# Kernel tuning notes

Measured on AMD Instinct MI355X. Metric: run time of the kernel, lower is better.

Reference implementation:

```python
import jax, jax.numpy as jnp
from jax import lax
import numpy as np

NEG = jnp.float32(-1e9)


def monotonic_alignment_search(logp, text_lengths, mel_lengths):
    """Glow-TTS style MAS. logp: [B, Tt, Tm] (log_softmax over text axis).
    Returns integer durations [B, Tt] summing to mel_lengths per batch."""
    B, Tt, Tm = logp.shape
    i_range = jnp.arange(Tt)
    text_mask = i_range[None, :] < text_lengths[:, None]            # [B, Tt]
    logp = jnp.where(text_mask[:, :, None], logp, NEG)

    # ---- forward DP over mel frames: Q[i,j] = logp[i,j] + max(Q[i,j-1], Q[i-1,j-1])
    q0 = jnp.where(i_range[None, :] == 0, logp[:, :, 0], NEG)        # [B, Tt]

    def fwd(q, lp_j):
        q_shift = jnp.concatenate([jnp.full((B, 1), NEG), q[:, :-1]], axis=1)
        take_diag = q_shift > q                                      # came from i-1
        q_new = lp_j + jnp.maximum(q, q_shift)
        return q_new, take_diag

    _, choices = lax.scan(fwd, q0, jnp.moveaxis(logp[:, :, 1:], 2, 0))  # [Tm-1, B, Tt]
    choices = jnp.concatenate([jnp.zeros((1, B, Tt), bool), choices], axis=0)  # align j

    # ---- backtrack from (text_len-1, mel_len-1) down to j=0
    b_idx = jnp.arange(B)

    def bwd(i, j):
        active = j < mel_lengths                                     # [B]
        dur_inc = (active[:, None] & (i_range[None, :] == i[:, None]))
        ch = choices[j, b_idx, i]                                    # [B] bool
        i_new = jnp.where(active & (j > 0), i - ch.astype(i.dtype), i)
        return i_new, dur_inc

    i0 = text_lengths - 1
    _, durs = lax.scan(bwd, i0, jnp.arange(Tm - 1, -1, -1))
    return durs.sum(0).astype(jnp.int32)                             # [B, Tt]


def length_regulate(h_text, durations, mel_lengths, Tm):
    """Expand h_text [B,Tt,D] by durations [B,Tt] to [B,Tm,D]."""
    B, Tt, D = h_text.shape
    cum = jnp.cumsum(durations, axis=1)                              # [B, Tt]
    j = jnp.arange(Tm)
    idx = (cum[:, None, :] <= j[None, :, None]).sum(-1)              # [B, Tm]
    idx = jnp.clip(idx, 0, Tt - 1)
    h_exp = jnp.take_along_axis(h_text, idx[:, :, None], axis=1)     # [B, Tm, D]
    mel_mask = j[None, :] < mel_lengths[:, None]
    return h_exp * mel_mask[:, :, None].astype(h_exp.dtype)


def setup_inputs() -> dict:
    B, Tt, Tm, D, M = 32, 512, 2048, 512, 80
    k = jax.random.split(jax.random.key(0), 6)
    return {
        "h_text": jax.random.normal(k[0], (B, Tt, D), jnp.float32),
        "mel": jax.random.normal(k[1], (B, M, Tm), jnp.float32),
        "text_lengths": jax.random.randint(k[2], (B,), 256, Tt + 1, jnp.int32),
        "mel_lengths": jax.random.randint(k[3], (B,), 1024, Tm + 1, jnp.int32),
        "w_proj": jax.random.normal(k[4], (D, M), jnp.float32) * 0.02,
        "b_proj": jnp.zeros((D,), jnp.float32),
        "log_dur_pred": jax.random.normal(k[5], (B, Tt), jnp.float32) * 0.5,
    }


def reference(h_text, mel, text_lengths, mel_lengths, w_proj, b_proj, log_dur_pred):
    B, Tt, D = h_text.shape
    Tm = mel.shape[2]

    # mel_proj = Linear(n_mels -> d_model) on mel.transpose(1,2)
    mel_proj = jnp.einsum('bmt,dm->btd', mel, w_proj) + b_proj       # [B, Tm, D]

    # alignment scores + masked log_softmax over text axis
    attn = jnp.einsum('btd,bsd->bts', h_text, mel_proj)              # [B, Tt, Tm]
    text_mask = jnp.arange(Tt)[None, :] >= text_lengths[:, None]
    mel_mask = jnp.arange(Tm)[None, :] >= mel_lengths[:, None]
    attn = jnp.where(text_mask[:, :, None], NEG, attn)
    attn = jnp.where(mel_mask[:, None, :], NEG, attn)
    logp = jax.nn.log_softmax(attn, axis=1)

    durations = monotonic_alignment_search(logp, text_lengths, mel_lengths)

    # duration loss (masked sum-MSE in log domain)
    dur_mask = (jnp.arange(Tt)[None, :] < text_lengths[:, None]).astype(jnp.float32)
    log_dur_gt = jnp.log(jnp.clip(durations.astype(jnp.float32), 1.0, None))
    diff = log_dur_pred * dur_mask - log_dur_gt * dur_mask
    dur_loss = jnp.sum(diff * diff) / jnp.sum(dur_mask)

    h_expanded = length_regulate(h_text, durations, mel_lengths, Tm)  # [B, Tm, D]
    return (h_expanded, dur_loss, durations)
```

## Files before the change

### kernel.cpp

```cpp
#include <hip/hip_runtime.h>
#include <math.h>

#define Bn 32
#define TT 512
#define TM 2048
#define DD 512
#define MMp 80
#define NEGF (-1.0e9f)

constexpr size_t LOSS_OFF = (size_t)Bn * TM * DD;
constexpr size_t DUR_OFF  = LOSS_OFF + 1;

__global__ __launch_bounds__(256) void k0_wtx(const float* __restrict__ w,
                                              const float* __restrict__ bias,
                                              float* __restrict__ wTx) {
    int m = blockIdx.x;
    for (int d = threadIdx.x; d < DD; d += 256) {
        float v = 0.f;
        if (m < 80) v = w[d * 80 + m];
        else if (m == 80) v = bias[d];
        wTx[m * DD + d] = v;
    }
}

__global__ __launch_bounds__(256) void k1_hw(const float* __restrict__ h_text,
                                             const float* __restrict__ wTx,
                                             float* __restrict__ hwX) {
    int bid = blockIdx.x;
    int b = bid >> 3;
    int i0 = (bid & 7) * 64;
    int t = threadIdx.x;
    int tr = t & 15, tc = t >> 4;
    __shared__ __align__(16) float Asub[64 * 68];
    __shared__ __align__(16) float Bsub[96 * 68];
    float acc[4][6];
#pragma unroll
    for (int a = 0; a < 4; ++a)
#pragma unroll
        for (int c = 0; c < 6; ++c) acc[a][c] = 0.f;

    for (int d0 = 0; d0 < DD; d0 += 64) {
        __syncthreads();
#pragma unroll
        for (int p = 0; p < 4; ++p) {
            int lin = p * 256 + t;
            int r = lin >> 4, dq = lin & 15;
            *(float4*)&Asub[r * 68 + dq * 4] =
                *(const float4*)&h_text[((size_t)(b * TT + i0 + r)) * DD + d0 + dq * 4];
        }
#pragma unroll
        for (int p = 0; p < 6; ++p) {
            int lin = p * 256 + t;
            int cc = lin >> 4, dq = lin & 15;
            *(float4*)&Bsub[cc * 68 + dq * 4] =
                *(const float4*)&wTx[(size_t)cc * DD + d0 + dq * 4];
        }
        __syncthreads();
#pragma unroll
        for (int dd = 0; dd < 16; ++dd) {
            float4 a[4], bb[6];
#pragma unroll
            for (int ri = 0; ri < 4; ++ri)
                a[ri] = *(const float4*)&Asub[(tr * 4 + ri) * 68 + dd * 4];
#pragma unroll
            for (int ci = 0; ci < 6; ++ci)
                bb[ci] = *(const float4*)&Bsub[(tc * 6 + ci) * 68 + dd * 4];
#pragma unroll
            for (int ri = 0; ri < 4; ++ri)
#pragma unroll
                for (int ci = 0; ci < 6; ++ci) {
                    acc[ri][ci] += a[ri].x * bb[ci].x;
                    acc[ri][ci] += a[ri].y * bb[ci].y;
                    acc[ri][ci] += a[ri].z * bb[ci].z;
                    acc[ri][ci] += a[ri].w * bb[ci].w;
                }
        }
    }
#pragma unroll
    for (int ri = 0; ri < 4; ++ri)
#pragma unroll
        for (int ci = 0; ci < 6; ++ci)
            hwX[((size_t)b * 96 + tc * 6 + ci) * DD + i0 + tr * 4 + ri] = acc[ri][ci];
}

__global__ __launch_bounds__(256) void k2_attn(const float* __restrict__ hwX,
                                               const float* __restrict__ mel,
                                               const int* __restrict__ tlen,
                                               const int* __restrict__ mlen,
                                               float* __restrict__ logpT) {
    const int b = blockIdx.y;
    const int ml = mlen[b];
    const int j0 = blockIdx.x * 32;
    if (j0 >= ml) return;
    const int tl = tlen[b];
    const int tid = threadIdx.x;
    const int ig = tid >> 2;
    const int jg = tid & 3;

    __shared__ __align__(16) float hwS[16 * 512];
    __shared__ __align__(16) float melS[16 * 32];
    __shared__ float red[32 * 64];
    __shared__ float colmax[32];
    __shared__ float lsum[32];

    float acc[8][8];
#pragma unroll
    for (int a = 0; a < 8; ++a)
#pragma unroll
        for (int c = 0; c < 8; ++c) acc[a][c] = 0.f;

    for (int mc = 0; mc < 80; mc += 16) {
        __syncthreads();
#pragma unroll
        for (int p = 0; p < 8; ++p) {
            int lin = p * 256 + tid;
            int mm = lin >> 7, iq = lin & 127;
            *(float4*)&hwS[mm * 512 + iq * 4] =
                *(const float4*)&hwX[((size_t)b * 96 + mc + mm) * DD + iq * 4];
        }
#pragma unroll
        for (int p = 0; p < 2; ++p) {
            int lin = p * 256 + tid;
            int mm = lin >> 5, jj = lin & 31;
            melS[lin] = mel[((size_t)b * 80 + mc + mm) * TM + j0 + jj];
        }
        __syncthreads();
#pragma unroll
        for (int mm = 0; mm < 16; ++mm) {
            float4 a0 = *(const float4*)&hwS[mm * 512 + ig * 8];
            float4 a1 = *(const float4*)&hwS[mm * 512 + ig * 8 + 4];
            float4 b0 = *(const float4*)&melS[mm * 32 + jg * 8];
            float4 b1 = *(const float4*)&melS[mm * 32 + jg * 8 + 4];
            float av[8] = {a0.x, a0.y, a0.z, a0.w, a1.x, a1.y, a1.z, a1.w};
            float bv[8] = {b0.x, b0.y, b0.z, b0.w, b1.x, b1.y, b1.z, b1.w};
#pragma unroll
            for (int ii = 0; ii < 8; ++ii)
#pragma unroll
                for (int jj = 0; jj < 8; ++jj) acc[ii][jj] += av[ii] * bv[jj];
        }
    }
    float4 h0 = *(const float4*)&hwX[((size_t)b * 96 + 80) * DD + ig * 8];
    float4 h1 = *(const float4*)&hwX[((size_t)b * 96 + 80) * DD + ig * 8 + 4];
    float hb[8] = {h0.x, h0.y, h0.z, h0.w, h1.x, h1.y, h1.z, h1.w};
#pragma unroll
    for (int ii = 0; ii < 8; ++ii) {
        bool valid = (ig * 8 + ii) < tl;
#pragma unroll
        for (int jj = 0; jj < 8; ++jj)
            acc[ii][jj] = valid ? (acc[ii][jj] + hb[ii]) : NEGF;
    }
    __syncthreads();
#pragma unroll
    for (int jj = 0; jj < 8; ++jj) {
        float m = acc[0][jj];
#pragma unroll
        for (int ii = 1; ii < 8; ++ii) m = fmaxf(m, acc[ii][jj]);
        red[(jg * 8 + jj) * 64 + ig] = m;
    }
    __syncthreads();
    if (tid < 32) {
        float m = red[tid * 64];
        for (int g = 1; g < 64; ++g) m = fmaxf(m, red[tid * 64 + g]);
        colmax[tid] = m;
    }
    __syncthreads();
#pragma unroll
    for (int jj = 0; jj < 8; ++jj) {
        float cm = colmax[jg * 8 + jj];
        float s = 0.f;
#pragma unroll
        for (int ii = 0; ii < 8; ++ii) s += expf(acc[ii][jj] - cm);
        red[(jg * 8 + jj) * 64 + ig] = s;
    }
    __syncthreads();
    if (tid < 32) {
        float s = 0.f;
        for (int g = 0; g < 64; ++g) s += red[tid * 64 + g];
        lsum[tid] = logf(s);
    }
    __syncthreads();
#pragma unroll
    for (int jj = 0; jj < 8; ++jj) {
        int j = j0 + jg * 8 + jj;
        if (j < ml) {
            float cm = colmax[jg * 8 + jj], ls = lsum[jg * 8 + jj];
            float o[8];
#pragma unroll
            for (int ii = 0; ii < 8; ++ii) {
                int i = ig * 8 + ii;
                o[ii] = (i < tl) ? ((acc[ii][jj] - cm) - ls) : NEGF;
            }
            float* dst = &logpT[((size_t)b * TM + j) * TT + ig * 8];
            *(float4*)dst = make_float4(o[0], o[1], o[2], o[3]);
            *(float4*)(dst + 4) = make_float4(o[4], o[5], o[6], o[7]);
        }
    }
}

#define BCOLS 15
#define NBATCH 137

__device__ __forceinline__ void lds_dma16(const float* g, float* l) {
    __builtin_amdgcn_global_load_lds((const __attribute__((address_space(1))) void*)g,
                                     (__attribute__((address_space(3))) void*)l,
                                     16, 0, 0);
}
#define WAITALL  asm volatile("s_waitcnt vmcnt(0)" ::: "memory")
#define WAITLGKM asm volatile("s_waitcnt lgkmcnt(0)" ::: "memory")

__device__ __forceinline__ float dpp_shr1(float old, float src) {
    return __int_as_float(__builtin_amdgcn_update_dpp(
        __float_as_int(old), __float_as_int(src), 0x138, 0xF, 0xF, false));
}

__global__ __launch_bounds__(64, 1) void k3_dp(const float* __restrict__ logpT,
                                               const int* __restrict__ tlen,
                                               const int* __restrict__ mlen,
                                               unsigned* __restrict__ gwords,
                                               int* __restrict__ idxmap,
                                               float* __restrict__ dOut) {
    const int b = blockIdx.x;
    const int lane = threadIdx.x;
    const int tl = tlen[b];
    const int ml = mlen[b];
    __shared__ __align__(16) float ring0[BCOLS * 512];
    __shared__ __align__(16) float ring1[BCOLS * 512];
    __shared__ int durs[TT];
#pragma unroll
    for (int k = 0; k < 8; ++k) durs[lane * 8 + k] = 0;

    const float* colbase = logpT + (size_t)b * TM * TT;
    unsigned* gwb = gwords + (size_t)b * TT * 64;

    float q[8];
    unsigned accb[8];
#pragma unroll
    for (int k = 0; k < 8; ++k) { q[k] = NEGF; accb[k] = 0u; }
    if (lane == 0) q[0] = colbase[0];

    {
        const float* g0 = colbase + (size_t)512 + lane * 4;
#pragma unroll
        for (int p = 0; p < BCOLS; ++p) {
            lds_dma16(g0 + p * 512,       &ring0[p * 512]);
            lds_dma16(g0 + p * 512 + 256, &ring0[p * 512 + 256]);
        }
    }
    WAITALL;

    unsigned* gp = gwb + lane * 8 * 64;
    int jj = 1;
    for (int n = 0; n < NBATCH; ++n) {
        const float* bufc = (n & 1) ? ring1 : ring0;
        float* bufn = (n & 1) ? ring0 : ring1;
        float4 ra[BCOLS], rb[BCOLS];
#pragma unroll
        for (int p = 0; p < BCOLS; ++p) {
            ra[p] = *(const float4*)&bufc[p * 512 + lane * 8];
            rb[p] = *(const float4*)&bufc[p * 512 + lane * 8 + 4];
        }
        WAITLGKM;
        if (n + 1 < NBATCH) {
            const int jb = 1 + (n + 1) * BCOLS;
#pragma unroll
            for (int p = 0; p < BCOLS; ++p) {
                int c = jb + p;
                c = (c > TM - 1) ? (TM - 1) : c;
                const float* g = colbase + (size_t)c * 512 + lane * 4;
                lds_dma16(g,       &bufn[p * 512]);
                lds_dma16(g + 256, &bufn[p * 512 + 256]);
            }
        }
#pragma unroll
        for (int p = 0; p < BCOLS; ++p) {
            float lp[8] = {ra[p].x, ra[p].y, ra[p].z, ra[p].w,
                           rb[p].x, rb[p].y, rb[p].z, rb[p].w};
            float nb[8];
            nb[0] = dpp_shr1(NEGF, q[7]);
#pragma unroll
            for (int k = 1; k < 8; ++k) nb[k] = q[k - 1];
            const unsigned m32 = 1u << (jj & 31);
#pragma unroll
            for (int k = 0; k < 8; ++k) {
                if (nb[k] > q[k]) accb[k] |= m32;
                q[k] = lp[k] + fmaxf(q[k], nb[k]);
            }
            if ((jj & 31) == 31) {
#pragma unroll
                for (int k = 0; k < 8; ++k) { gp[k * 64] = accb[k]; accb[k] = 0u; }
                gp += 1;
            }
            ++jj;
        }
        WAITALL;
    }
    __threadfence();
    __syncthreads();

    {
        int i = tl - 1;
        int j = ml - 1;
        unsigned r0, r1, r2, r3, r4, r5, r6, r7;
        {
            int a0 = tl - 1, a1 = tl - 2, a2 = tl - 3, a3 = tl - 4;
            int a4 = tl - 5, a5 = tl - 6, a6 = tl - 7, a7 = tl - 8;
            a1 = a1 < 0 ? 0 : a1; a2 = a2 < 0 ? 0 : a2; a3 = a3 < 0 ? 0 : a3;
            a4 = a4 < 0 ? 0 : a4; a5 = a5 < 0 ? 0 : a5; a6 = a6 < 0 ? 0 : a6;
            a7 = a7 < 0 ? 0 : a7;
            r0 = gwb[a0 * 64 + lane]; r1 = gwb[a1 * 64 + lane];
            r2 = gwb[a2 * 64 + lane]; r3 = gwb[a3 * 64 + lane];
            r4 = gwb[a4 * 64 + lane]; r5 = gwb[a5 * 64 + lane];
            r6 = gwb[a6 * 64 + lane]; r7 = gwb[a7 * 64 + lane];
        }
        int nf = tl - 9;
        int guard = TT + 2;
        while (guard-- > 0) {
            unsigned w = r0;
            r0 = r1; r1 = r2; r2 = r3; r3 = r4; r4 = r5; r5 = r6; r6 = r7;
            {
                int rf = (nf < 0) ? 0 : nf;
                r7 = gwb[rf * 64 + lane];
                --nf;
            }
            int jw = j >> 5, rr = j & 31;
            unsigned topmask = (rr == 31) ? 0xFFFFFFFFu : ((1u << (rr + 1)) - 1u);
            unsigned wm = (lane < jw) ? w : ((lane == jw) ? (w & topmask) : 0u);
            unsigned long long bal = __ballot(wm != 0u);
            if (bal == 0ull) {
                if (lane == 0) durs[i] = j + 1;
                break;
            }
            int hl = 63 - __clzll(bal);
            unsigned whl = (unsigned)__builtin_amdgcn_readlane((int)wm, hl);
            int jp = (hl << 5) + (31 - __clz(whl));
            if (lane == 0) durs[i] = j - jp + 1;
            j = jp - 1;
            if (--i < 0) break;
        }
    }
    __syncthreads();

    int d[8], pre[8];
    int run = 0;
#pragma unroll
    for (int k = 0; k < 8; ++k) { d[k] = durs[lane * 8 + k]; pre[k] = run; run += d[k]; }
    int v = run;
#pragma unroll
    for (int off = 1; off < 64; off <<= 1) {
        int n = __shfl_up(v, off);
        if (lane >= off) v += n;
    }
    int base = v - run;
#pragma unroll
    for (int k = 0; k < 8; ++k) {
        int i = lane * 8 + k;
        dOut[DUR_OFF + (size_t)b * TT + i] = (float)d[k];
        int st = base + pre[k];
        for (int t2 = 0; t2 < d[k]; ++t2) idxmap[b * TM + st + t2] = i;
    }
}

__global__ __launch_bounds__(128) void k4_expand(const float* __restrict__ h_text,
                                                 const int* __restrict__ idxmap,
                                                 const int* __restrict__ mlen,
                                                 float* __restrict__ dOut) {
    int bid = blockIdx.x;
    int b = bid >> 11;
    int j = bid & (TM - 1);
    int t = threadIdx.x;
    float4* orow = (float4*)dOut + (size_t)bid * 128;
    if (j < mlen[b]) {
        int i = idxmap[bid];
        const float4* hrow = (const float4*)h_text + ((size_t)(b * TT + i)) * 128;
        orow[t] = hrow[t];
    } else {
        orow[t] = make_float4(0.f, 0.f, 0.f, 0.f);
    }
}

__global__ __launch_bounds__(256) void k5_loss(const float* __restrict__ pred,
                                               const int* __restrict__ tlen,
                                               float* __restrict__ dOut) {
    __shared__ float rs[256];
    __shared__ int rc[256];
    int t = threadIdx.x;
    float s = 0.f;
    int c = 0;
    for (int idx = t; idx < Bn * TT; idx += 256) {
        int b = idx >> 9, i = idx & 511;
        if (i < tlen[b]) {
            float dv = dOut[DUR_OFF + idx];
            float lg = logf(fmaxf(dv, 1.0f));
            float df = pred[idx] - lg;
            s += df * df;
            c += 1;
        }
    }
    rs[t] = s; rc[t] = c;
    __syncthreads();
    for (int off = 128; off > 0; off >>= 1) {
        if (t < off) { rs[t] += rs[t + off]; rc[t] += rc[t + off]; }
        __syncthreads();
    }
    if (t == 0) dOut[LOSS_OFF] = rs[0] / (float)rc[0];
}

extern "C" void kernel_launch(void* const* d_in, const int* in_sizes, int n_in,
                              void* d_out, int out_size, void* d_ws, size_t ws_size,
                              hipStream_t stream) {
    const float* h_text = (const float*)d_in[0];
    const float* mel    = (const float*)d_in[1];
    const int*   tlen   = (const int*)d_in[2];
    const int*   mlen   = (const int*)d_in[3];
    const float* w      = (const float*)d_in[4];
    const float* bias   = (const float*)d_in[5];
    const float* pred   = (const float*)d_in[6];
    float* out = (float*)d_out;

    float*    logpT  = (float*)d_ws;
    float*    hwX    = logpT + (size_t)Bn * TM * TT;
    float*    wTx    = hwX + (size_t)Bn * 96 * DD;
    unsigned* gwords = (unsigned*)(wTx + 96 * DD);
    int*      idxmap = (int*)(gwords + (size_t)Bn * TT * 64);

    k0_wtx<<<dim3(96), dim3(256), 0, stream>>>(w, bias, wTx);
    k1_hw<<<dim3(256), dim3(256), 0, stream>>>(h_text, wTx, hwX);
    k2_attn<<<dim3(64, 32), dim3(256), 0, stream>>>(hwX, mel, tlen, mlen, logpT);
    k3_dp<<<dim3(32), dim3(64), 0, stream>>>(logpT, tlen, mlen, gwords, idxmap, out);
    k4_expand<<<dim3(Bn * TM), dim3(128), 0, stream>>>(h_text, idxmap, mlen, out);
    k5_loss<<<dim3(1), dim3(256), 0, stream>>>(pred, tlen, out);
}
```

Baseline: 827.9 us.

## Replace LDS DMA double buffer with register triple-buffered global loads in DP

The forward DP kernel used to stage logp columns through two LDS ring buffers filled by global_load_lds DMA, with explicit vmcnt and lgkmcnt waits. It now loads each column batch straight from global memory into three rotating register buffers, issuing two batches ahead of the one being consumed, with 8 columns per batch instead of 15. This removes the LDS round trip and the full vmcnt wait at the end of every batch, so the serial recurrence should stall less on memory. In exchange register pressure rises, and the old clamp on column indices is gone, so prefetches run past column TM-1 into the next batch's data or past the end of the buffer for the last batch.

```diff
diff --git a/kernel.cpp b/kernel.cpp
--- a/kernel.cpp
+++ b/kernel.cpp
@@ -197,16 +197,8 @@
     }
 }
 
-#define BCOLS 15
-#define NBATCH 137
-
-__device__ __forceinline__ void lds_dma16(const float* g, float* l) {
-    __builtin_amdgcn_global_load_lds((const __attribute__((address_space(1))) void*)g,
-                                     (__attribute__((address_space(3))) void*)l,
-                                     16, 0, 0);
-}
-#define WAITALL  asm volatile("s_waitcnt vmcnt(0)" ::: "memory")
-#define WAITLGKM asm volatile("s_waitcnt lgkmcnt(0)" ::: "memory")
+#define BCOLS 8
+#define NBATCH 258
 
 __device__ __forceinline__ float dpp_shr1(float old, float src) {
     return __int_as_float(__builtin_amdgcn_update_dpp(
@@ -223,8 +215,6 @@
     const int lane = threadIdx.x;
     const int tl = tlen[b];
     const int ml = mlen[b];
-    __shared__ __align__(16) float ring0[BCOLS * 512];
-    __shared__ __align__(16) float ring1[BCOLS * 512];
     __shared__ int durs[TT];
 #pragma unroll
     for (int k = 0; k < 8; ++k) durs[lane * 8 + k] = 0;
@@ -238,62 +228,60 @@
     for (int k = 0; k < 8; ++k) { q[k] = NEGF; accb[k] = 0u; }
     if (lane == 0) q[0] = colbase[0];
 
-    {
-        const float* g0 = colbase + (size_t)512 + lane * 4;
-#pragma unroll
-        for (int p = 0; p < BCOLS; ++p) {
-            lds_dma16(g0 + p * 512,       &ring0[p * 512]);
-            lds_dma16(g0 + p * 512 + 256, &ring0[p * 512 + 256]);
-        }
-    }
-    WAITALL;
-
     unsigned* gp = gwb + lane * 8 * 64;
     int jj = 1;
-    for (int n = 0; n < NBATCH; ++n) {
-        const float* bufc = (n & 1) ? ring1 : ring0;
-        float* bufn = (n & 1) ? ring0 : ring1;
-        float4 ra[BCOLS], rb[BCOLS];
-#pragma unroll
-        for (int p = 0; p < BCOLS; ++p) {
-            ra[p] = *(const float4*)&bufc[p * 512 + lane * 8];
-            rb[p] = *(const float4*)&bufc[p * 512 + lane * 8 + 4];
-        }
-        WAITLGKM;
-        if (n + 1 < NBATCH) {
-            const int jb = 1 + (n + 1) * BCOLS;
-#pragma unroll
-            for (int p = 0; p < BCOLS; ++p) {
-                int c = jb + p;
-                c = (c > TM - 1) ? (TM - 1) : c;
-                const float* g = colbase + (size_t)c * 512 + lane * 4;
-                lds_dma16(g,       &bufn[p * 512]);
-                lds_dma16(g + 256, &bufn[p * 512 + 256]);
-            }
-        }
-#pragma unroll
-        for (int p = 0; p < BCOLS; ++p) {
-            float lp[8] = {ra[p].x, ra[p].y, ra[p].z, ra[p].w,
-                           rb[p].x, rb[p].y, rb[p].z, rb[p].w};
-            float nb[8];
-            nb[0] = dpp_shr1(NEGF, q[7]);
-#pragma unroll
-            for (int k = 1; k < 8; ++k) nb[k] = q[k - 1];
-            const unsigned m32 = 1u << (jj & 31);
-#pragma unroll
-            for (int k = 0; k < 8; ++k) {
-                if (nb[k] > q[k]) accb[k] |= m32;
-                q[k] = lp[k] + fmaxf(q[k], nb[k]);
-            }
-            if ((jj & 31) == 31) {
-#pragma unroll
-                for (int k = 0; k < 8; ++k) { gp[k * 64] = accb[k]; accb[k] = 0u; }
-                gp += 1;
-            }
-            ++jj;
-        }
-        WAITALL;
-    }
+    const float* lanebase = colbase + lane * 8;
+
+    float4 ra0[BCOLS], rb0[BCOLS], ra1[BCOLS], rb1[BCOLS], ra2[BCOLS], rb2[BCOLS];
+
+#define ISSUE(nb_, ra_, rb_) do {                                              \
+        const float* g_ = lanebase + ((size_t)(1 + (nb_) * BCOLS)) * 512;      \
+        _Pragma("unroll")                                                      \
+        for (int p_ = 0; p_ < BCOLS; ++p_) {                                   \
+            ra_[p_] = *(const float4*)(g_ + (size_t)p_ * 512);                 \
+            rb_[p_] = *(const float4*)(g_ + (size_t)p_ * 512 + 4);             \
+        }                                                                      \
+    } while (0)
+
+#define STEPS(ra_, rb_) do {                                                   \
+        _Pragma("unroll")                                                      \
+        for (int p_ = 0; p_ < BCOLS; ++p_) {                                   \
+            float lp_[8] = {ra_[p_].x, ra_[p_].y, ra_[p_].z, ra_[p_].w,        \
+                            rb_[p_].x, rb_[p_].y, rb_[p_].z, rb_[p_].w};       \
+            float nb_[8];                                                      \
+            nb_[0] = dpp_shr1(NEGF, q[7]);                                     \
+            _Pragma("unroll")                                                  \
+            for (int k_ = 1; k_ < 8; ++k_) nb_[k_] = q[k_ - 1];                \
+            const unsigned m32_ = 1u << (jj & 31);                             \
+            _Pragma("unroll")                                                  \
+            for (int k_ = 0; k_ < 8; ++k_) {                                   \
+                if (nb_[k_] > q[k_]) accb[k_] |= m32_;                         \
+                q[k_] = lp_[k_] + fmaxf(q[k_], nb_[k_]);                       \
+            }                                                                  \
+            if ((jj & 31) == 31) {                \
+                _Pragma("unroll")                                              \
+                for (int k_ = 0; k_ < 8; ++k_) {                               \
+                    gp[k_ * 64] = accb[k_]; accb[k_] = 0u;                     \
+                }                                                              \
+                gp += 1;                                                       \
+            }                                                                  \
+            ++jj;                                                              \
+        }                                                                      \
+    } while (0)
+
+    ISSUE(0, ra0, rb0);
+    ISSUE(1, ra1, rb1);
+    for (int n = 0; n < NBATCH; n += 3) {
+        ISSUE(n + 2, ra2, rb2);
+        STEPS(ra0, rb0);
+        ISSUE(n + 3, ra0, rb0);
+        STEPS(ra1, rb1);
+        ISSUE(n + 4, ra1, rb1);
+        STEPS(ra2, rb2);
+    }
+#undef ISSUE
+#undef STEPS
+
     __threadfence();
     __syncthreads();
 
```

Measured after the change: 752.6 us. 1.1x faster.

## Split MAS DP into producer wave for LDS prefetch and compute wave

Applied to the files above, without the earlier changes.

The DP kernel now runs two waves per batch. One wave issues global-to-LDS DMA loads for the next 16 columns while the other does the forward recurrence. Each compute lane now owns rows split as two groups of 4 (lane*4 and 256+lane*4), with a DPP rotate to carry the boundary between the halves. The aim is to take memory waits off the serial DP critical path, at the cost of a __syncthreads per 16-column block. The backtrack and idxmap writes also gain bounds clamping, and k4 masks the index.

```diff
diff --git a/kernel.cpp b/kernel.cpp
--- a/kernel.cpp
+++ b/kernel.cpp
@@ -197,166 +197,184 @@
     }
 }
 
-#define BCOLS 15
-#define NBATCH 137
+#define KVB 16
+#define NKB 128
+
+typedef float vf4 __attribute__((ext_vector_type(4)));
 
 __device__ __forceinline__ void lds_dma16(const float* g, float* l) {
     __builtin_amdgcn_global_load_lds((const __attribute__((address_space(1))) void*)g,
                                      (__attribute__((address_space(3))) void*)l,
                                      16, 0, 0);
 }
-#define WAITALL  asm volatile("s_waitcnt vmcnt(0)" ::: "memory")
-#define WAITLGKM asm volatile("s_waitcnt lgkmcnt(0)" ::: "memory")
 
 __device__ __forceinline__ float dpp_shr1(float old, float src) {
     return __int_as_float(__builtin_amdgcn_update_dpp(
         __float_as_int(old), __float_as_int(src), 0x138, 0xF, 0xF, false));
 }
-
-__global__ __launch_bounds__(64, 1) void k3_dp(const float* __restrict__ logpT,
-                                               const int* __restrict__ tlen,
-                                               const int* __restrict__ mlen,
-                                               unsigned* __restrict__ gwords,
-                                               int* __restrict__ idxmap,
-                                               float* __restrict__ dOut) {
+__device__ __forceinline__ float dpp_ror1(float src) {
+    return __int_as_float(__builtin_amdgcn_update_dpp(
+        __float_as_int(src), __float_as_int(src), 0x13C, 0xF, 0xF, false));
+}
+
+__global__ __launch_bounds__(128, 1) void k3_dp(const float* __restrict__ logpT,
+                                                const int* __restrict__ tlen,
+                                                const int* __restrict__ mlen,
+                                                unsigned* __restrict__ gwords,
+                                                int* __restrict__ idxmap,
+                                                float* __restrict__ dOut) {
     const int b = blockIdx.x;
-    const int lane = threadIdx.x;
+    const int tid = threadIdx.x;
+    const int wid = tid >> 6;
+    const int lane = tid & 63;
     const int tl = tlen[b];
     const int ml = mlen[b];
-    __shared__ __align__(16) float ring0[BCOLS * 512];
-    __shared__ __align__(16) float ring1[BCOLS * 512];
+
+    __shared__ __align__(16) float ring[2][KVB][512];
     __shared__ int durs[TT];
-#pragma unroll
-    for (int k = 0; k < 8; ++k) durs[lane * 8 + k] = 0;
+    for (int idx = tid; idx < TT; idx += 128) durs[idx] = 0;
 
     const float* colbase = logpT + (size_t)b * TM * TT;
     unsigned* gwb = gwords + (size_t)b * TT * 64;
 
-    float q[8];
-    unsigned accb[8];
-#pragma unroll
-    for (int k = 0; k < 8; ++k) { q[k] = NEGF; accb[k] = 0u; }
-    if (lane == 0) q[0] = colbase[0];
-
-    {
-        const float* g0 = colbase + (size_t)512 + lane * 4;
-#pragma unroll
-        for (int p = 0; p < BCOLS; ++p) {
-            lds_dma16(g0 + p * 512,       &ring0[p * 512]);
-            lds_dma16(g0 + p * 512 + 256, &ring0[p * 512 + 256]);
-        }
-    }
-    WAITALL;
-
-    unsigned* gp = gwb + lane * 8 * 64;
+    if (wid == 1) {
+        const float* src0 = colbase + (size_t)512 + lane * 4;
+#pragma unroll
+        for (int c = 0; c < KVB; ++c) {
+            lds_dma16(src0 + c * 512,       &ring[0][c][0]);
+            lds_dma16(src0 + c * 512 + 256, &ring[0][c][256]);
+        }
+    }
+
+    float qa[4], qb[4];
+    unsigned accA[4], accB[4];
+#pragma unroll
+    for (int k = 0; k < 4; ++k) { qa[k] = NEGF; qb[k] = NEGF; accA[k] = 0u; accB[k] = 0u; }
+    if (wid == 0 && lane == 0) qa[0] = colbase[0];
+    unsigned* gpA = gwb + (size_t)(4 * lane) * 64;
+    unsigned* gpB = gwb + (size_t)(256 + 4 * lane) * 64;
+    int woff = 0;
     int jj = 1;
-    for (int n = 0; n < NBATCH; ++n) {
-        const float* bufc = (n & 1) ? ring1 : ring0;
-        float* bufn = (n & 1) ? ring0 : ring1;
-        float4 ra[BCOLS], rb[BCOLS];
-#pragma unroll
-        for (int p = 0; p < BCOLS; ++p) {
-            ra[p] = *(const float4*)&bufc[p * 512 + lane * 8];
-            rb[p] = *(const float4*)&bufc[p * 512 + lane * 8 + 4];
-        }
-        WAITLGKM;
-        if (n + 1 < NBATCH) {
-            const int jb = 1 + (n + 1) * BCOLS;
-#pragma unroll
-            for (int p = 0; p < BCOLS; ++p) {
-                int c = jb + p;
-                c = (c > TM - 1) ? (TM - 1) : c;
-                const float* g = colbase + (size_t)c * 512 + lane * 4;
-                lds_dma16(g,       &bufn[p * 512]);
-                lds_dma16(g + 256, &bufn[p * 512 + 256]);
+    const int lane4 = lane * 4;
+
+    __syncthreads();
+
+    for (int kb = 0; kb < NKB; ++kb) {
+        if (wid == 1) {
+            if (kb + 1 < NKB) {
+                const int j0 = 1 + (kb + 1) * KVB;
+                const float* src = colbase + (size_t)j0 * 512 + lane * 4;
+                float* slot = &ring[(kb + 1) & 1][0][0];
+#pragma unroll
+                for (int c = 0; c < KVB; ++c) {
+                    lds_dma16(src + c * 512,       slot + c * 512);
+                    lds_dma16(src + c * 512 + 256, slot + c * 512 + 256);
+                }
             }
-        }
-#pragma unroll
-        for (int p = 0; p < BCOLS; ++p) {
-            float lp[8] = {ra[p].x, ra[p].y, ra[p].z, ra[p].w,
-                           rb[p].x, rb[p].y, rb[p].z, rb[p].w};
-            float nb[8];
-            nb[0] = dpp_shr1(NEGF, q[7]);
-#pragma unroll
-            for (int k = 1; k < 8; ++k) nb[k] = q[k - 1];
-            const unsigned m32 = 1u << (jj & 31);
-#pragma unroll
-            for (int k = 0; k < 8; ++k) {
-                if (nb[k] > q[k]) accb[k] |= m32;
-                q[k] = lp[k] + fmaxf(q[k], nb[k]);
+        } else {
+            const float* slab = &ring[kb & 1][0][0];
+#pragma unroll
+            for (int c = 0; c < KVB; ++c) {
+                vf4 la = *(const vf4*)&slab[c * 512 + lane4];
+                vf4 lb = *(const vf4*)&slab[c * 512 + 256 + lane4];
+                float wrap = dpp_ror1(qa[3]);
+                float nA0 = dpp_shr1(NEGF, qa[3]);
+                float nB0 = dpp_shr1(wrap, qb[3]);
+                float nA[4], nB[4];
+                nA[0] = nA0; nB[0] = nB0;
+#pragma unroll
+                for (int k = 1; k < 4; ++k) { nA[k] = qa[k - 1]; nB[k] = qb[k - 1]; }
+                const unsigned m32 = 1u << (jj & 31);
+                float lpA[4] = {la[0], la[1], la[2], la[3]};
+                float lpB[4] = {lb[0], lb[1], lb[2], lb[3]};
+#pragma unroll
+                for (int k = 0; k < 4; ++k) {
+                    if (nA[k] > qa[k]) accA[k] |= m32;
+                    qa[k] = lpA[k] + fmaxf(qa[k], nA[k]);
+                    if (nB[k] > qb[k]) accB[k] |= m32;
+                    qb[k] = lpB[k] + fmaxf(qb[k], nB[k]);
+                }
+                if ((jj & 31) == 31) {
+#pragma unroll
+                    for (int k = 0; k < 4; ++k) {
+                        gpA[k * 64 + woff] = accA[k]; accA[k] = 0u;
+                        gpB[k * 64 + woff] = accB[k]; accB[k] = 0u;
+                    }
+                    ++woff;
+                }
+                ++jj;
             }
-            if ((jj & 31) == 31) {
-#pragma unroll
-                for (int k = 0; k < 8; ++k) { gp[k * 64] = accb[k]; accb[k] = 0u; }
-                gp += 1;
+        }
+        __syncthreads();
+    }
+
+    __threadfence();
+    __syncthreads();
+
+    if (wid == 0) {
+        {
+            int i = tl - 1;
+            int j = ml - 1;
+            unsigned r0, r1, r2, r3, r4, r5, r6, r7;
+            {
+                int a0 = tl - 1, a1 = tl - 2, a2 = tl - 3, a3 = tl - 4;
+                int a4 = tl - 5, a5 = tl - 6, a6 = tl - 7, a7 = tl - 8;
+                a1 = a1 < 0 ? 0 : a1; a2 = a2 < 0 ? 0 : a2; a3 = a3 < 0 ? 0 : a3;
+                a4 = a4 < 0 ? 0 : a4; a5 = a5 < 0 ? 0 : a5; a6 = a6 < 0 ? 0 : a6;
+                a7 = a7 < 0 ? 0 : a7;
+                r0 = gwb[a0 * 64 + lane]; r1 = gwb[a1 * 64 + lane];
+                r2 = gwb[a2 * 64 + lane]; r3 = gwb[a3 * 64 + lane];
+                r4 = gwb[a4 * 64 + lane]; r5 = gwb[a5 * 64 + lane];
+                r6 = gwb[a6 * 64 + lane]; r7 = gwb[a7 * 64 + lane];
             }
-            ++jj;
-        }
-        WAITALL;
-    }
-    __threadfence();
-    __syncthreads();
-
-    {
-        int i = tl - 1;
-        int j = ml - 1;
-        unsigned r0, r1, r2, r3, r4, r5, r6, r7;
-        {
-            int a0 = tl - 1, a1 = tl - 2, a2 = tl - 3, a3 = tl - 4;
-            int a4 = tl - 5, a5 = tl - 6, a6 = tl - 7, a7 = tl - 8;
-            a1 = a1 < 0 ? 0 : a1; a2 = a2 < 0 ? 0 : a2; a3 = a3 < 0 ? 0 : a3;
-            a4 = a4 < 0 ? 0 : a4; a5 = a5 < 0 ? 0 : a5; a6 = a6 < 0 ? 0 : a6;
-            a7 = a7 < 0 ? 0 : a7;
-            r0 = gwb[a0 * 64 + lane]; r1 = gwb[a1 * 64 + lane];
-            r2 = gwb[a2 * 64 + lane]; r3 = gwb[a3 * 64 + lane];
-            r4 = gwb[a4 * 64 + lane]; r5 = gwb[a5 * 64 + lane];
-            r6 = gwb[a6 * 64 + lane]; r7 = gwb[a7 * 64 + lane];
-        }
-        int nf = tl - 9;
-        int guard = TT + 2;
-        while (guard-- > 0) {
-            unsigned w = r0;
-            r0 = r1; r1 = r2; r2 = r3; r3 = r4; r4 = r5; r5 = r6; r6 = r7;
-            {
-                int rf = (nf < 0) ? 0 : nf;
-                r7 = gwb[rf * 64 + lane];
-                --nf;
+            int nf = tl - 9;
+            int guard = TT + 2;
+            while (guard-- > 0) {
+                unsigned w = r0;
+                r0 = r1; r1 = r2; r2 = r3; r3 = r4; r4 = r5; r5 = r6; r6 = r7;
+                {
+                    int rf = (nf < 0) ? 0 : nf;
+                    r7 = gwb[rf * 64 + lane];
+                    --nf;
+                }
+                int jw = j >> 5, rr = j & 31;
+                unsigned topmask = (rr == 31) ? 0xFFFFFFFFu : ((1u << (rr + 1)) - 1u);
+                unsigned wm = (lane < jw) ? w : ((lane == jw) ? (w & topmask) : 0u);
+                unsigned long long bal = __ballot(wm != 0u);
+                if (bal == 0ull) {
+                    if (lane == 0) durs[i] = j + 1;
+                    break;
+                }
+                int hl = 63 - __clzll(bal);
+                unsigned whl = (unsigned)__builtin_amdgcn_readlane((int)wm, hl);
+                int jp = (hl << 5) + (31 - __clz(whl));
+                if (lane == 0) durs[i] = j - jp + 1;
+                j = jp - 1;
+                if (--i < 0) break;
             }
-            int jw = j >> 5, rr = j & 31;
-            unsigned topmask = (rr == 31) ? 0xFFFFFFFFu : ((1u << (rr + 1)) - 1u);
-            unsigned wm = (lane < jw) ? w : ((lane == jw) ? (w & topmask) : 0u);
-            unsigned long long bal = __ballot(wm != 0u);
-            if (bal == 0ull) {
-                if (lane == 0) durs[i] = j + 1;
-                break;
-            }
-            int hl = 63 - __clzll(bal);
-            unsigned whl = (unsigned)__builtin_amdgcn_readlane((int)wm, hl);
-            int jp = (hl << 5) + (31 - __clz(whl));
-            if (lane == 0) durs[i] = j - jp + 1;
-            j = jp - 1;
-            if (--i < 0) break;
-        }
-    }
-    __syncthreads();
-
-    int d[8], pre[8];
-    int run = 0;
-#pragma unroll
-    for (int k = 0; k < 8; ++k) { d[k] = durs[lane * 8 + k]; pre[k] = run; run += d[k]; }
-    int v = run;
-#pragma unroll
-    for (int off = 1; off < 64; off <<= 1) {
-        int n = __shfl_up(v, off);
-        if (lane >= off) v += n;
-    }
-    int base = v - run;
-#pragma unroll
-    for (int k = 0; k < 8; ++k) {
-        int i = lane * 8 + k;
-        dOut[DUR_OFF + (size_t)b * TT + i] = (float)d[k];
-        int st = base + pre[k];
-        for (int t2 = 0; t2 < d[k]; ++t2) idxmap[b * TM + st + t2] = i;
+        }
+
+        int d[8], pre[8];
+        int run = 0;
+#pragma unroll
+        for (int k = 0; k < 8; ++k) { d[k] = durs[lane * 8 + k]; pre[k] = run; run += d[k]; }
+        int v = run;
+#pragma unroll
+        for (int off = 1; off < 64; off <<= 1) {
+            int n = __shfl_up(v, off);
+            if (lane >= off) v += n;
+        }
+        int base = v - run;
+#pragma unroll
+        for (int k = 0; k < 8; ++k) {
+            int i = lane * 8 + k;
+            dOut[DUR_OFF + (size_t)b * TT + i] = (float)d[k];
+            int st = base + pre[k];
+            int en = st + d[k];
+            if (en > TM) en = TM;
+            if (st < 0) st = 0;
+            for (int t2 = st; t2 < en; ++t2) idxmap[b * TM + t2] = i;
+        }
     }
 }
 
@@ -370,7 +388,7 @@
     int t = threadIdx.x;
     float4* orow = (float4*)dOut + (size_t)bid * 128;
     if (j < mlen[b]) {
-        int i = idxmap[bid];
+        int i = idxmap[bid] & (TT - 1);
         const float4* hrow = (const float4*)h_text + ((size_t)(b * TT + i)) * 128;
         orow[t] = hrow[t];
     } else {
@@ -426,7 +444,7 @@
     k0_wtx<<<dim3(96), dim3(256), 0, stream>>>(w, bias, wTx);
     k1_hw<<<dim3(256), dim3(256), 0, stream>>>(h_text, wTx, hwX);
     k2_attn<<<dim3(64, 32), dim3(256), 0, stream>>>(hwX, mel, tlen, mlen, logpT);
-    k3_dp<<<dim3(32), dim3(64), 0, stream>>>(logpT, tlen, mlen, gwords, idxmap, out);
+    k3_dp<<<dim3(32), dim3(128), 0, stream>>>(logpT, tlen, mlen, gwords, idxmap, out);
     k4_expand<<<dim3(Bn * TM), dim3(128), 0, stream>>>(h_text, idxmap, mlen, out);
     k5_loss<<<dim3(1), dim3(256), 0, stream>>>(pred, tlen, out);
 }
```

Result: no change. 829.5 us (+0.2%).

## Rotate DP across three wavefronts with register-prefetched column chunks

Applied to the files above, without the earlier changes.

The serial MAS forward DP kernel now runs three wavefronts per batch. Each wavefront owns every third chunk of 16 mel columns and prefetches its next chunk straight into registers with global loads, replacing the LDS DMA ring. The DP state (q and partial choice bits) is handed between waves through shared memory, with a block barrier after each chunk, so memory latency is hidden by the other waves' loads. This adds a barrier and an LDS state round trip per chunk, and clamps the idxmap range and index as safety.

```diff
diff --git a/kernel.cpp b/kernel.cpp
--- a/kernel.cpp
+++ b/kernel.cpp
@@ -197,166 +197,179 @@
     }
 }
 
-#define BCOLS 15
-#define NBATCH 137
-
-__device__ __forceinline__ void lds_dma16(const float* g, float* l) {
-    __builtin_amdgcn_global_load_lds((const __attribute__((address_space(1))) void*)g,
-                                     (__attribute__((address_space(3))) void*)l,
-                                     16, 0, 0);
-}
-#define WAITALL  asm volatile("s_waitcnt vmcnt(0)" ::: "memory")
-#define WAITLGKM asm volatile("s_waitcnt lgkmcnt(0)" ::: "memory")
+#define KC3 16
+#define NB3 128
+#define K3T 192
+
+typedef float vf4 __attribute__((ext_vector_type(4)));
+typedef unsigned vu4 __attribute__((ext_vector_type(4)));
+
+#define SB0() __builtin_amdgcn_sched_barrier(0)
 
 __device__ __forceinline__ float dpp_shr1(float old, float src) {
     return __int_as_float(__builtin_amdgcn_update_dpp(
         __float_as_int(old), __float_as_int(src), 0x138, 0xF, 0xF, false));
 }
 
-__global__ __launch_bounds__(64, 1) void k3_dp(const float* __restrict__ logpT,
-                                               const int* __restrict__ tlen,
-                                               const int* __restrict__ mlen,
-                                               unsigned* __restrict__ gwords,
-                                               int* __restrict__ idxmap,
-                                               float* __restrict__ dOut) {
+__global__ __launch_bounds__(K3T, 1) void k3_dp(const float* __restrict__ logpT,
+                                                const int* __restrict__ tlen,
+                                                const int* __restrict__ mlen,
+                                                unsigned* __restrict__ gwords,
+                                                int* __restrict__ idxmap,
+                                                float* __restrict__ dOut) {
     const int b = blockIdx.x;
-    const int lane = threadIdx.x;
+    const int tid = threadIdx.x;
+    const int wid = tid >> 6;
+    const int lane = tid & 63;
     const int tl = tlen[b];
     const int ml = mlen[b];
-    __shared__ __align__(16) float ring0[BCOLS * 512];
-    __shared__ __align__(16) float ring1[BCOLS * 512];
+
+    __shared__ __align__(16) float qs[TT];
+    __shared__ __align__(16) unsigned as2[TT];
     __shared__ int durs[TT];
-#pragma unroll
-    for (int k = 0; k < 8; ++k) durs[lane * 8 + k] = 0;
-
+    for (int idx = tid; idx < TT; idx += K3T) {
+        durs[idx] = 0;
+        qs[idx] = NEGF;
+        as2[idx] = 0u;
+    }
     const float* colbase = logpT + (size_t)b * TM * TT;
     unsigned* gwb = gwords + (size_t)b * TT * 64;
-
-    float q[8];
-    unsigned accb[8];
-#pragma unroll
-    for (int k = 0; k < 8; ++k) { q[k] = NEGF; accb[k] = 0u; }
-    if (lane == 0) q[0] = colbase[0];
-
-    {
-        const float* g0 = colbase + (size_t)512 + lane * 4;
-#pragma unroll
-        for (int p = 0; p < BCOLS; ++p) {
-            lds_dma16(g0 + p * 512,       &ring0[p * 512]);
-            lds_dma16(g0 + p * 512 + 256, &ring0[p * 512 + 256]);
-        }
-    }
-    WAITALL;
-
-    unsigned* gp = gwb + lane * 8 * 64;
-    int jj = 1;
-    for (int n = 0; n < NBATCH; ++n) {
-        const float* bufc = (n & 1) ? ring1 : ring0;
-        float* bufn = (n & 1) ? ring0 : ring1;
-        float4 ra[BCOLS], rb[BCOLS];
-#pragma unroll
-        for (int p = 0; p < BCOLS; ++p) {
-            ra[p] = *(const float4*)&bufc[p * 512 + lane * 8];
-            rb[p] = *(const float4*)&bufc[p * 512 + lane * 8 + 4];
-        }
-        WAITLGKM;
-        if (n + 1 < NBATCH) {
-            const int jb = 1 + (n + 1) * BCOLS;
-#pragma unroll
-            for (int p = 0; p < BCOLS; ++p) {
-                int c = jb + p;
-                c = (c > TM - 1) ? (TM - 1) : c;
-                const float* g = colbase + (size_t)c * 512 + lane * 4;
-                lds_dma16(g,       &bufn[p * 512]);
-                lds_dma16(g + 256, &bufn[p * 512 + 256]);
+    if (tid == 0) qs[0] = colbase[0];
+
+    const float* lanebase = colbase + lane * 8;
+
+    vf4 ba[KC3], bbv[KC3];
+
+#define ISSUE3(nb_) do {                                                       \
+        const float* g_ = lanebase + ((size_t)(1 + (nb_) * KC3)) * 512;        \
+        _Pragma("unroll")                                                      \
+        for (int p_ = 0; p_ < KC3; ++p_) {                                     \
+            ba[p_]  = *(const vf4*)(g_ + (size_t)p_ * 512);                    \
+            bbv[p_] = *(const vf4*)(g_ + (size_t)p_ * 512 + 4);                \
+        }                                                                      \
+    } while (0)
+
+    ISSUE3(wid);
+    __syncthreads();
+
+    for (int n = 0; n < NB3; ++n) {
+        if (wid == (n % 3)) {
+            vf4 q0v = *(const vf4*)&qs[8 * lane];
+            vf4 q1v = *(const vf4*)&qs[8 * lane + 4];
+            vu4 a0v = *(const vu4*)&as2[8 * lane];
+            vu4 a1v = *(const vu4*)&as2[8 * lane + 4];
+            float q[8] = {q0v[0], q0v[1], q0v[2], q0v[3],
+                          q1v[0], q1v[1], q1v[2], q1v[3]};
+            unsigned accb[8] = {a0v[0], a0v[1], a0v[2], a0v[3],
+                                a1v[0], a1v[1], a1v[2], a1v[3]};
+            int jj = 1 + n * KC3;
+            unsigned* gp = gwb + (size_t)lane * 8 * 64
+                         + ((unsigned)(KC3 * n + 1) >> 5);
+#pragma unroll
+            for (int p = 0; p < KC3; ++p) {
+                float lp[8] = {ba[p][0], ba[p][1], ba[p][2], ba[p][3],
+                               bbv[p][0], bbv[p][1], bbv[p][2], bbv[p][3]};
+                float nb[8];
+                nb[0] = dpp_shr1(NEGF, q[7]);
+#pragma unroll
+                for (int k = 1; k < 8; ++k) nb[k] = q[k - 1];
+                const unsigned m32 = 1u << (jj & 31);
+#pragma unroll
+                for (int k = 0; k < 8; ++k) {
+                    if (nb[k] > q[k]) accb[k] |= m32;
+                    q[k] = lp[k] + fmaxf(q[k], nb[k]);
+                }
+                if ((jj & 31) == 31) {
+#pragma unroll
+                    for (int k = 0; k < 8; ++k) { gp[k * 64] = accb[k]; accb[k] = 0u; }
+                    gp += 1;
+                }
+                ++jj;
             }
-        }
-#pragma unroll
-        for (int p = 0; p < BCOLS; ++p) {
-            float lp[8] = {ra[p].x, ra[p].y, ra[p].z, ra[p].w,
-                           rb[p].x, rb[p].y, rb[p].z, rb[p].w};
-            float nb[8];
-            nb[0] = dpp_shr1(NEGF, q[7]);
-#pragma unroll
-            for (int k = 1; k < 8; ++k) nb[k] = q[k - 1];
-            const unsigned m32 = 1u << (jj & 31);
-#pragma unroll
-            for (int k = 0; k < 8; ++k) {
-                if (nb[k] > q[k]) accb[k] |= m32;
-                q[k] = lp[k] + fmaxf(q[k], nb[k]);
+            vf4 wq0 = {q[0], q[1], q[2], q[3]};
+            vf4 wq1 = {q[4], q[5], q[6], q[7]};
+            vu4 wa0 = {accb[0], accb[1], accb[2], accb[3]};
+            vu4 wa1 = {accb[4], accb[5], accb[6], accb[7]};
+            *(vf4*)&qs[8 * lane] = wq0;
+            *(vf4*)&qs[8 * lane + 4] = wq1;
+            *(vu4*)&as2[8 * lane] = wa0;
+            *(vu4*)&as2[8 * lane + 4] = wa1;
+        }
+        asm volatile("s_waitcnt lgkmcnt(0)" ::: "memory");
+        SB0();
+        __builtin_amdgcn_s_barrier();
+        SB0();
+        if (wid == (n % 3) && n + 3 < NB3) ISSUE3(n + 3);
+    }
+#undef ISSUE3
+
+    __threadfence();
+    __syncthreads();
+
+    if (wid == 0) {
+        {
+            int i = tl - 1;
+            int j = ml - 1;
+            unsigned r0, r1, r2, r3, r4, r5, r6, r7;
+            {
+                int a0 = tl - 1, a1 = tl - 2, a2 = tl - 3, a3 = tl - 4;
+                int a4 = tl - 5, a5 = tl - 6, a6 = tl - 7, a7 = tl - 8;
+                a1 = a1 < 0 ? 0 : a1; a2 = a2 < 0 ? 0 : a2; a3 = a3 < 0 ? 0 : a3;
+                a4 = a4 < 0 ? 0 : a4; a5 = a5 < 0 ? 0 : a5; a6 = a6 < 0 ? 0 : a6;
+                a7 = a7 < 0 ? 0 : a7;
+                r0 = gwb[a0 * 64 + lane]; r1 = gwb[a1 * 64 + lane];
+                r2 = gwb[a2 * 64 + lane]; r3 = gwb[a3 * 64 + lane];
+                r4 = gwb[a4 * 64 + lane]; r5 = gwb[a5 * 64 + lane];
+                r6 = gwb[a6 * 64 + lane]; r7 = gwb[a7 * 64 + lane];
             }
-            if ((jj & 31) == 31) {
-#pragma unroll
-                for (int k = 0; k < 8; ++k) { gp[k * 64] = accb[k]; accb[k] = 0u; }
-                gp += 1;
+            int nf = tl - 9;
+            int guard = TT + 2;
+            while (guard-- > 0) {
+                unsigned w = r0;
+                r0 = r1; r1 = r2; r2 = r3; r3 = r4; r4 = r5; r5 = r6; r6 = r7;
+                {
+                    int rf = (nf < 0) ? 0 : nf;
+                    r7 = gwb[rf * 64 + lane];
+                    --nf;
+                }
+                int jw = j >> 5, rr = j & 31;
+                unsigned topmask = (rr == 31) ? 0xFFFFFFFFu : ((1u << (rr + 1)) - 1u);
+                unsigned wm = (lane < jw) ? w : ((lane == jw) ? (w & topmask) : 0u);
+                unsigned long long bal = __ballot(wm != 0u);
+                if (bal == 0ull) {
+                    if (lane == 0) durs[i] = j + 1;
+                    break;
+                }
+                int hl = 63 - __clzll(bal);
+                unsigned whl = (unsigned)__builtin_amdgcn_readlane((int)wm, hl);
+                int jp = (hl << 5) + (31 - __clz(whl));
+                if (lane == 0) durs[i] = j - jp + 1;
+                j = jp - 1;
+                if (--i < 0) break;
             }
-            ++jj;
-        }
-        WAITALL;
-    }
-    __threadfence();
-    __syncthreads();
-
-    {
-        int i = tl - 1;
-        int j = ml - 1;
-        unsigned r0, r1, r2, r3, r4, r5, r6, r7;
-        {
-            int a0 = tl - 1, a1 = tl - 2, a2 = tl - 3, a3 = tl - 4;
-            int a4 = tl - 5, a5 = tl - 6, a6 = tl - 7, a7 = tl - 8;
-            a1 = a1 < 0 ? 0 : a1; a2 = a2 < 0 ? 0 : a2; a3 = a3 < 0 ? 0 : a3;
-            a4 = a4 < 0 ? 0 : a4; a5 = a5 < 0 ? 0 : a5; a6 = a6 < 0 ? 0 : a6;
-            a7 = a7 < 0 ? 0 : a7;
-            r0 = gwb[a0 * 64 + lane]; r1 = gwb[a1 * 64 + lane];
-            r2 = gwb[a2 * 64 + lane]; r3 = gwb[a3 * 64 + lane];
-            r4 = gwb[a4 * 64 + lane]; r5 = gwb[a5 * 64 + lane];
-            r6 = gwb[a6 * 64 + lane]; r7 = gwb[a7 * 64 + lane];
-        }
-        int nf = tl - 9;
-        int guard = TT + 2;
-        while (guard-- > 0) {
-            unsigned w = r0;
-            r0 = r1; r1 = r2; r2 = r3; r3 = r4; r4 = r5; r5 = r6; r6 = r7;
-            {
-                int rf = (nf < 0) ? 0 : nf;
-                r7 = gwb[rf * 64 + lane];
-                --nf;
-            }
-            int jw = j >> 5, rr = j & 31;
-            unsigned topmask = (rr == 31) ? 0xFFFFFFFFu : ((1u << (rr + 1)) - 1u);
-            unsigned wm = (lane < jw) ? w : ((lane == jw) ? (w & topmask) : 0u);
-            unsigned long long bal = __ballot(wm != 0u);
-            if (bal == 0ull) {
-                if (lane == 0) durs[i] = j + 1;
-                break;
-            }
-            int hl = 63 - __clzll(bal);
-            unsigned whl = (unsigned)__builtin_amdgcn_readlane((int)wm, hl);
-            int jp = (hl << 5) + (31 - __clz(whl));
-            if (lane == 0) durs[i] = j - jp + 1;
-            j = jp - 1;
-            if (--i < 0) break;
-        }
-    }
-    __syncthreads();
-
-    int d[8], pre[8];
-    int run = 0;
-#pragma unroll
-    for (int k = 0; k < 8; ++k) { d[k] = durs[lane * 8 + k]; pre[k] = run; run += d[k]; }
-    int v = run;
-#pragma unroll
-    for (int off = 1; off < 64; off <<= 1) {
-        int n = __shfl_up(v, off);
-        if (lane >= off) v += n;
-    }
-    int base = v - run;
-#pragma unroll
-    for (int k = 0; k < 8; ++k) {
-        int i = lane * 8 + k;
-        dOut[DUR_OFF + (size_t)b * TT + i] = (float)d[k];
-        int st = base + pre[k];
-        for (int t2 = 0; t2 < d[k]; ++t2) idxmap[b * TM + st + t2] = i;
+        }
+
+        int d[8], pre[8];
+        int run = 0;
+#pragma unroll
+        for (int k = 0; k < 8; ++k) { d[k] = durs[lane * 8 + k]; pre[k] = run; run += d[k]; }
+        int v = run;
+#pragma unroll
+        for (int off = 1; off < 64; off <<= 1) {
+            int nn = __shfl_up(v, off);
+            if (lane >= off) v += nn;
+        }
+        int base = v - run;
+#pragma unroll
+        for (int k = 0; k < 8; ++k) {
+            int i = lane * 8 + k;
+            dOut[DUR_OFF + (size_t)b * TT + i] = (float)d[k];
+            int st = base + pre[k];
+            int en = st + d[k];
+            if (en > TM) en = TM;
+            if (st < 0) st = 0;
+            for (int t2 = st; t2 < en; ++t2) idxmap[b * TM + t2] = i;
+        }
     }
 }
 
@@ -370,7 +383,7 @@
     int t = threadIdx.x;
     float4* orow = (float4*)dOut + (size_t)bid * 128;
     if (j < mlen[b]) {
-        int i = idxmap[bid];
+        int i = idxmap[bid] & (TT - 1);
         const float4* hrow = (const float4*)h_text + ((size_t)(b * TT + i)) * 128;
         orow[t] = hrow[t];
     } else {
@@ -426,7 +439,7 @@
     k0_wtx<<<dim3(96), dim3(256), 0, stream>>>(w, bias, wTx);
     k1_hw<<<dim3(256), dim3(256), 0, stream>>>(h_text, wTx, hwX);
     k2_attn<<<dim3(64, 32), dim3(256), 0, stream>>>(hwX, mel, tlen, mlen, logpT);
-    k3_dp<<<dim3(32), dim3(64), 0, stream>>>(logpT, tlen, mlen, gwords, idxmap, out);
+    k3_dp<<<dim3(32), dim3(K3T), 0, stream>>>(logpT, tlen, mlen, gwords, idxmap, out);
     k4_expand<<<dim3(Bn * TM), dim3(128), 0, stream>>>(h_text, idxmap, mlen, out);
     k5_loss<<<dim3(1), dim3(256), 0, stream>>>(pred, tlen, out);
 }
```

Result: faster. 741.6 us (-10.4%).
